# Optimization experiments

Measured on AMD Instinct MI355X. Metric: run time of the kernel, lower is better.

The kernel has to match this reference:

```python
import jax, jax.numpy as jnp
import numpy as np

B, S, HID, NH, HD = 2, 2048, 768, 12, 64
WINDOW = 128           # ModernBERT local attention window
ROPE_THETA = 10000.0   # local_rope_theta (layer_index=0 -> is_local_attention=True)


def _rotate_half(x):
    x1, x2 = jnp.split(x, 2, axis=-1)
    return jnp.concatenate([-x2, x1], axis=-1)


def setup_inputs() -> dict:
    key = jax.random.key(0)
    k1, k2, k3 = jax.random.split(key, 3)
    hidden_embed = jax.random.normal(k1, (B, S, HID), dtype=jnp.float32)
    Wq = jax.random.normal(k2, (HID, HID), dtype=jnp.float32) * (HID ** -0.5)
    Wo = jax.random.normal(k3, (HID, HID), dtype=jnp.float32) * (HID ** -0.5)
    position_index = jnp.arange(S, dtype=jnp.int32).reshape(1, S)
    # sliding-window additive mask: 0 inside window, -inf outside
    i = jnp.arange(S)
    dist = jnp.abs(i[:, None] - i[None, :])
    local_attention_mask = jnp.where(dist <= WINDOW // 2, 0.0, -jnp.inf).astype(jnp.float32)[None, None]
    global_attention_mask = jnp.zeros((1, 1, S, S), dtype=jnp.float32)
    return {
        "hidden_embed": hidden_embed,
        "Wq": Wq,
        "Wo": Wo,
        "local_attention_mask": local_attention_mask,
        "global_attention_mask": global_attention_mask,
        "position_index": position_index,
    }


def reference(hidden_embed, Wq, Wo, local_attention_mask, global_attention_mask, position_index):
    # q projection; NOTE: source has k = q.view(...), v = q.view(...) -> k and v ARE q
    q = hidden_embed @ Wq.T                                  # [B,S,HID]
    q = q.reshape(B, S, NH, HD).transpose(0, 2, 1, 3)        # [B,NH,S,HD]

    # RoPE
    inv_freq = 1.0 / (ROPE_THETA ** (jnp.arange(0, HD, 2, dtype=jnp.float32) / HD))  # [HD/2]
    pos = position_index.reshape(-1).astype(jnp.float32)     # [S]
    freqs = pos[:, None] * inv_freq[None, :]                 # [S,HD/2]
    emb = jnp.concatenate([freqs, freqs], axis=-1)           # [S,HD]
    cos, sin = jnp.cos(emb), jnp.sin(emb)
    q_rot = q * cos + _rotate_half(q) * sin                  # [B,NH,S,HD]
    k_rot = q_rot                                            # k == q before rope -> same after rope
    v = q                                                    # v == q (no rope on v)

    # masked SDPA (local layer -> local sliding-window mask)
    scale = jnp.asarray(HD, jnp.float32) ** -0.5
    scores = jnp.einsum('bhtd,bhsd->bhts', q_rot, k_rot) * scale + local_attention_mask
    attn = jax.nn.softmax(scores, axis=-1)                   # [B,NH,S,S]
    out = jnp.einsum('bhts,bhsd->bhtd', attn, v)             # [B,NH,S,HD]
    out = out.transpose(0, 2, 1, 3).reshape(B, S, HID)
    return out @ Wo.T
```

## Files before the change

### kernel.cpp

```cpp
#include <hip/hip_runtime.h>
#include <hip/hip_bf16.h>
#include <math.h>
#include <stdint.h>

#define B_    2
#define S_    2048
#define HID_  768
#define NH_   12
#define HD_   64
#define NROWS (B_ * S_)
#define N_HID_ELEM (NROWS * HID_)
#define N_W_ELEM   (HID_ * HID_)

#define KW   224
#define KSTR 232

#define TAB_ELEMS (S_ * 32)

typedef __bf16 bf16x8 __attribute__((ext_vector_type(8)));
typedef float  floatx4 __attribute__((ext_vector_type(4)));

__global__ void convert_inputs_kernel(const float* __restrict__ src_hidden,
                                      const float* __restrict__ src_w1,
                                      const float* __restrict__ src_w2,
                                      const int*   __restrict__ pos_idx,
                                      __hip_bfloat16* __restrict__ Hb,
                                      __hip_bfloat16* __restrict__ Wqb,
                                      __hip_bfloat16* __restrict__ Wob,
                                      float2* __restrict__ tab)
{
    int i = blockIdx.x * blockDim.x + threadIdx.x;
    const int NH4 = N_HID_ELEM / 4, NW4 = N_W_ELEM / 4;
    const int total4 = NH4 + 2 * NW4;
    if (i < total4) {
        const float* src;
        __hip_bfloat16* dst;
        int off;
        if (i < NH4)           { src = src_hidden; dst = Hb;  off = i; }
        else if (i < NH4+NW4)  { src = src_w1;     dst = Wqb; off = i - NH4; }
        else                   { src = src_w2;     dst = Wob; off = i - NH4 - NW4; }
        float4 v = reinterpret_cast<const float4*>(src)[off];
        __hip_bfloat16 o[4] = { __float2bfloat16(v.x), __float2bfloat16(v.y),
                                __float2bfloat16(v.z), __float2bfloat16(v.w) };
        *reinterpret_cast<uint64_t*>(dst + 4 * (size_t)off) = *reinterpret_cast<uint64_t*>(o);
    } else {
        int t = i - total4;
        if (t < TAB_ELEMS) {
            int s = t >> 5, f = t & 31;
            float inv = exp2f((float)f * (-0.41524101186092024f));
            float sn, cs;
            sincosf((float)pos_idx[s] * inv, &sn, &cs);
            tab[t] = make_float2(cs, sn);
        }
    }
}

__device__ __forceinline__ void gload_lds16(const __hip_bfloat16* g, __hip_bfloat16* l)
{
    __builtin_amdgcn_global_load_lds(
        (const __attribute__((address_space(1))) void*)g,
        (__attribute__((address_space(3))) void*)l, 16, 0, 0);
}

template<int ROPE>
__global__ __launch_bounds__(512) void gemm64k2(
    const __hip_bfloat16* __restrict__ A,
    const __hip_bfloat16* __restrict__ W,
    __hip_bfloat16* __restrict__ C,
    __hip_bfloat16* __restrict__ C2,
    float* __restrict__ Cf,
    const float2* __restrict__ tab,
    int M, int N, int K)
{
    __shared__ __align__(16) __hip_bfloat16 Ald[2][2][2][64][32];
    __shared__ __align__(16) __hip_bfloat16 Wld[2][2][2][64][32];

    const int tid  = threadIdx.x;
    const int kg   = tid >> 8;
    const int wv4  = (tid >> 6) & 3;
    const int lane = tid & 63;
    const int l16  = lane & 15;
    const int quad = lane >> 4;
    const int m0 = blockIdx.x * 64;
    const int n0 = blockIdx.y * 64;

    const int c    = wv4 * 64 + lane;
    const int sr   = c >> 2;
    const int sc8  = ((c & 3) ^ ((sr >> 1) & 3)) * 8;
    const int kbase = kg * 384;

    const __hip_bfloat16* gA = A + (size_t)(m0 + sr) * K + kbase + sc8;
    const __hip_bfloat16* gW = W + (size_t)(n0 + sr) * K + kbase + sc8;

    floatx4 acc[4] = {};
    const int ra  = wv4 * 16 + l16;
    const int qsw = (quad ^ ((l16 >> 1) & 3)) * 8;

#define STAGE(itx, buf) do {                                          \
        const int ko_ = (itx) * 64;                                   \
        gload_lds16(gA + ko_,      &Ald[kg][buf][0][wv4 * 16][0]);    \
        gload_lds16(gA + ko_ + 32, &Ald[kg][buf][1][wv4 * 16][0]);    \
        gload_lds16(gW + ko_,      &Wld[kg][buf][0][wv4 * 16][0]);    \
        gload_lds16(gW + ko_ + 32, &Wld[kg][buf][1][wv4 * 16][0]);    \
    } while (0)

    STAGE(0, 0);
    STAGE(1, 1);

#pragma unroll
    for (int it = 0; it < 6; ++it) {
        const int cur = it & 1;
        if (it == 5) { asm volatile("s_waitcnt vmcnt(0)" ::: "memory"); }
        else         { asm volatile("s_waitcnt vmcnt(4)" ::: "memory"); }
        __builtin_amdgcn_s_barrier();
        __builtin_amdgcn_sched_barrier(0);
#pragma unroll
        for (int ks = 0; ks < 2; ++ks) {
            bf16x8 a = *reinterpret_cast<const bf16x8*>(&Ald[kg][cur][ks][ra][qsw]);
#pragma unroll
            for (int u = 0; u < 4; ++u) {
                bf16x8 w = *reinterpret_cast<const bf16x8*>(
                    &Wld[kg][cur][ks][u * 16 + l16][qsw]);
                acc[u] = __builtin_amdgcn_mfma_f32_16x16x32_bf16(a, w, acc[u], 0, 0, 0);
            }
        }
        __builtin_amdgcn_sched_barrier(0);
        __builtin_amdgcn_s_barrier();
        if (it + 2 < 6) STAGE(it + 2, cur);
    }
#undef STAGE

    __syncthreads();
    float* Red = reinterpret_cast<float*>(&Ald[0][0][0][0][0]);
    if (kg == 1) {
#pragma unroll
        for (int u = 0; u < 4; ++u)
#pragma unroll
            for (int r = 0; r < 4; ++r)
                Red[(wv4 * 16 + quad * 4 + r) * 68 + u * 16 + l16] = acc[u][r];
    }
    __syncthreads();
    if (kg == 1) return;
#pragma unroll
    for (int u = 0; u < 4; ++u)
#pragma unroll
        for (int r = 0; r < 4; ++r)
            acc[u][r] += Red[(wv4 * 16 + quad * 4 + r) * 68 + u * 16 + l16];

    if (ROPE) {
#pragma unroll
        for (int r = 0; r < 4; ++r) {
            int m = m0 + wv4 * 16 + quad * 4 + r;
            int s = m & (S_ - 1);
#pragma unroll
            for (int u = 0; u < 2; ++u) {
                float2 cssn = tab[s * 32 + u * 16 + l16];
                float cs = cssn.x, sn = cssn.y;
                float q0 = acc[u][r];
                float q1 = acc[u + 2][r];
                size_t base = (size_t)m * HID_ + n0 + u * 16 + l16;
                C [base]      = __float2bfloat16(q0);
                C [base + 32] = __float2bfloat16(q1);
                C2[base]      = __float2bfloat16(q0 * cs - q1 * sn);
                C2[base + 32] = __float2bfloat16(q1 * cs + q0 * sn);
            }
        }
    } else {
#pragma unroll
        for (int u = 0; u < 4; ++u)
#pragma unroll
            for (int r = 0; r < 4; ++r) {
                int row = m0 + wv4 * 16 + quad * 4 + r;
                int col = n0 + u * 16 + l16;
                Cf[(size_t)row * N + col] = acc[u][r];
            }
    }
}

__global__ __launch_bounds__(256) void attn_kernel(
    const __hip_bfloat16* __restrict__ Q,
    const __hip_bfloat16* __restrict__ Qr,
    __hip_bfloat16* __restrict__ O)
{
    __shared__ __align__(16) __hip_bfloat16 Vt[64][KSTR];
    __shared__ __align__(16) __hip_bfloat16 KP[64 * KSTR];

    const int bh = blockIdx.y;
    const int b  = bh / NH_;
    const int h  = bh % NH_;
    const int i0 = blockIdx.x * 64;
    const int tid = threadIdx.x;

    if (tid < KW) {
        int j  = i0 - 64 + tid;
        int jc = min(max(j, 0), S_ - 1);
        const __hip_bfloat16* vrow = Q + ((size_t)(b * S_ + jc)) * HID_ + h * HD_;
#pragma unroll
        for (int d8i = 0; d8i < 8; ++d8i) {
            bf16x8 v = *reinterpret_cast<const bf16x8*>(vrow + d8i * 8);
            const __hip_bfloat16* ve = reinterpret_cast<const __hip_bfloat16*>(&v);
#pragma unroll
            for (int e = 0; e < 8; ++e) Vt[d8i * 8 + e][tid] = ve[e];
        }
    }

    {
        const int wvb = (tid >> 6) * 64;
        const int ln  = tid & 63;
#pragma unroll
        for (int i = 0; i < 7; ++i) {
            int cbase = i * 256 + wvb;
            int cc  = cbase + ln;
            int row = cc >> 3;
            int gp  = cc & 7;
            int gl  = gp ^ (row & 7);
            int j   = i0 - 64 + row;
            int jc  = min(max(j, 0), S_ - 1);
            gload_lds16(Qr + ((size_t)(b * S_ + jc)) * HID_ + h * HD_ + gl * 8,
                        KP + (size_t)cbase * 8);
        }
    }
    __syncthreads();

    const int wv   = tid >> 6;
    const int lane = tid & 63;
    const int l16  = lane & 15;
    const int quad = lane >> 4;

    floatx4 sc[10] = {};
    const __hip_bfloat16* qrow =
        Qr + ((size_t)(b * S_ + i0 + wv * 16 + l16)) * HID_ + h * HD_ + quad * 8;
    __builtin_amdgcn_s_setprio(1);
#pragma unroll
    for (int ks = 0; ks < 2; ++ks) {
        bf16x8 a = *reinterpret_cast<const bf16x8*>(qrow + ks * 32);
#pragma unroll
        for (int t = 0; t < 10; ++t) {
            int w  = (wv + t) * 16 + l16;
            int gp = ((ks * 4 + quad) ^ (w & 7)) * 8;
            bf16x8 bfr = *reinterpret_cast<const bf16x8*>(&KP[w * 64 + gp]);
            sc[t] = __builtin_amdgcn_mfma_f32_16x16x32_bf16(a, bfr, sc[t], 0, 0, 0);
        }
    }
    __builtin_amdgcn_s_setprio(0);
    __syncthreads();

    const float scale = 0.125f;
    float denom[4];
#pragma unroll
    for (int r = 0; r < 4; ++r) {
        const int R = wv * 16 + quad * 4 + r;
        float xv[10];
        float mx = -3.0e38f;
#pragma unroll
        for (int t = 0; t < 10; ++t) {
            int w = (wv + t) * 16 + l16;
            int j = i0 - 64 + w;
            bool valid = (w >= R) && (w <= R + 128) && (j >= 0) && (j < S_);
            float x = valid ? sc[t][r] * scale : -1.0e30f;
            xv[t] = x;
            mx = fmaxf(mx, x);
        }
#pragma unroll
        for (int msk = 1; msk < 16; msk <<= 1) mx = fmaxf(mx, __shfl_xor(mx, msk, 64));
        float sum = 0.f;
#pragma unroll
        for (int t = 0; t < 10; ++t) {
            float p = __expf(xv[t] - mx);
            sum += p;
            KP[R * KSTR + (wv + t) * 16 + l16] = __float2bfloat16(p);
        }
#pragma unroll
        for (int msk = 1; msk < 16; msk <<= 1) sum += __shfl_xor(sum, msk, 64);
        denom[r] = sum;
    }
    __syncthreads();

    floatx4 oacc[4] = {};
    __builtin_amdgcn_s_setprio(1);
#pragma unroll
    for (int c = 0; c < 5; ++c) {
        const int base = wv * 16 + c * 32;
        bf16x8 a = *reinterpret_cast<const bf16x8*>(
            &KP[(wv * 16 + l16) * KSTR + base + quad * 8]);
#pragma unroll
        for (int u = 0; u < 4; ++u) {
            bf16x8 bfr = *reinterpret_cast<const bf16x8*>(&Vt[u * 16 + l16][base + quad * 8]);
            oacc[u] = __builtin_amdgcn_mfma_f32_16x16x32_bf16(a, bfr, oacc[u], 0, 0, 0);
        }
    }
    __builtin_amdgcn_s_setprio(0);

    __syncthreads();
    float* Of = reinterpret_cast<float*>(&KP[0]);
#pragma unroll
    for (int u = 0; u < 4; ++u)
#pragma unroll
        for (int r = 0; r < 4; ++r)
            Of[(wv * 16 + quad * 4 + r) * 68 + u * 16 + l16] = oacc[u][r] / denom[r];
    __syncthreads();
    {
        int row = tid >> 2;
        int seg = (tid & 3) * 16;
        __hip_bfloat16 ob[16];
#pragma unroll
        for (int e = 0; e < 16; ++e)
            ob[e] = __float2bfloat16(Of[row * 68 + seg + e]);
        __hip_bfloat16* dst = O + ((size_t)(b * S_ + i0 + row)) * HID_ + h * HD_ + seg;
        *reinterpret_cast<bf16x8*>(dst)     = *reinterpret_cast<bf16x8*>(ob);
        *reinterpret_cast<bf16x8*>(dst + 8) = *reinterpret_cast<bf16x8*>(ob + 8);
    }
}

extern "C" void kernel_launch(void* const* d_in, const int* in_sizes, int n_in,
                              void* d_out, int out_size, void* d_ws, size_t ws_size,
                              hipStream_t stream)
{
    int ih = -1, iw1 = -1, iw2 = -1, ip = -1;
    for (int i = 0; i < n_in; ++i) {
        int s = in_sizes[i];
        if      (s == N_HID_ELEM && ih < 0) ih = i;
        else if (s == N_W_ELEM)  { if (iw1 < 0) iw1 = i; else if (iw2 < 0) iw2 = i; }
        else if (s == S_ && ip < 0) ip = i;
    }
    if (ih < 0)  ih = 0;
    if (iw1 < 0) iw1 = 1;
    if (iw2 < 0) iw2 = 2;
    if (ip < 0)  ip = 5;

    const float* hidden = (const float*)d_in[ih];
    const float* w1     = (const float*)d_in[iw1];
    const float* w2     = (const float*)d_in[iw2];
    const int*   pos    = (const int*)d_in[ip];

    __hip_bfloat16* Hb  = (__hip_bfloat16*)d_ws;
    __hip_bfloat16* Wqb = Hb  + N_HID_ELEM;
    __hip_bfloat16* Wob = Wqb + N_W_ELEM;
    __hip_bfloat16* Q   = Wob + N_W_ELEM;
    __hip_bfloat16* Qr  = Q   + N_HID_ELEM;
    float2*         Tab = reinterpret_cast<float2*>(Qr + N_HID_ELEM);
    __hip_bfloat16* AO  = Hb;

    int conv4 = (N_HID_ELEM + 2 * N_W_ELEM) / 4;
    int convtot = conv4 + TAB_ELEMS;
    convert_inputs_kernel<<<(convtot + 255) / 256, 256, 0, stream>>>(
        hidden, w1, w2, pos, Hb, Wqb, Wob, Tab);

    dim3 gblk(NROWS / 64, HID_ / 64);

    gemm64k2<1><<<gblk, 512, 0, stream>>>(Hb, Wqb, Q, Qr, nullptr, Tab,
                                          NROWS, HID_, HID_);

    attn_kernel<<<dim3(S_ / 64, B_ * NH_), 256, 0, stream>>>(Q, Qr, AO);

    gemm64k2<0><<<gblk, 512, 0, stream>>>(AO, Wob, nullptr, nullptr, (float*)d_out,
                                          nullptr, NROWS, HID_, HID_);
}
```

Measured before the change: 137.9 us.

## Fuse all stages into one cooperative persistent kernel with 128x64 GEMM tiles

Replaces the four separate launches (convert, QKV GEMM+RoPE, attention, output GEMM) with a single cooperative kernel of 384 blocks that uses grid.sync between stages, and falls back to separate launches if the cooperative launch fails. The GEMM tile is reworked from a 64x64 tile with a 2-way split-K reduction to a 128x64 tile over the full K with XOR-swizzled LDS, which removes the LDS reduction step. The aim is to cut launch gaps and the reduction cost. In exchange the kernel pays for grid-wide barriers, runs with fewer blocks per stage and may see lower occupancy from the larger shared-memory footprint.

```diff
diff --git a/kernel.cpp b/kernel.cpp
--- a/kernel.cpp
+++ b/kernel.cpp
@@ -1,7 +1,10 @@
 #include <hip/hip_runtime.h>
 #include <hip/hip_bf16.h>
+#include <hip/hip_cooperative_groups.h>
 #include <math.h>
 #include <stdint.h>
+
+namespace cg = cooperative_groups;
 
 #define B_    2
 #define S_    2048
@@ -17,35 +20,48 @@
 
 #define TAB_ELEMS (S_ * 32)
 
+#define GRID_FUSED 384
+
 typedef __bf16 bf16x8 __attribute__((ext_vector_type(8)));
 typedef float  floatx4 __attribute__((ext_vector_type(4)));
 
-__global__ void convert_inputs_kernel(const float* __restrict__ src_hidden,
-                                      const float* __restrict__ src_w1,
-                                      const float* __restrict__ src_w2,
-                                      const int*   __restrict__ pos_idx,
-                                      __hip_bfloat16* __restrict__ Hb,
-                                      __hip_bfloat16* __restrict__ Wqb,
-                                      __hip_bfloat16* __restrict__ Wob,
-                                      float2* __restrict__ tab)
-{
-    int i = blockIdx.x * blockDim.x + threadIdx.x;
+__device__ __forceinline__ void gload_lds16(const __hip_bfloat16* g, __hip_bfloat16* l)
+{
+    __builtin_amdgcn_global_load_lds(
+        (const __attribute__((address_space(1))) void*)g,
+        (__attribute__((address_space(3))) void*)l, 16, 0, 0);
+}
+
+__device__ __forceinline__ floatx4 mfma16(bf16x8 a, bf16x8 b, floatx4 c)
+{
+    return __builtin_amdgcn_mfma_f32_16x16x32_bf16(a, b, c, 0, 0, 0);
+}
+
+__device__ __forceinline__ void convert_body(
+    int gtid, int gstride,
+    const float* __restrict__ src_hidden, const float* __restrict__ src_w1,
+    const float* __restrict__ src_w2, const int* __restrict__ pos_idx,
+    __hip_bfloat16* __restrict__ Hb, __hip_bfloat16* __restrict__ Wqb,
+    __hip_bfloat16* __restrict__ Wob, float2* __restrict__ tab)
+{
     const int NH4 = N_HID_ELEM / 4, NW4 = N_W_ELEM / 4;
     const int total4 = NH4 + 2 * NW4;
-    if (i < total4) {
-        const float* src;
-        __hip_bfloat16* dst;
-        int off;
-        if (i < NH4)           { src = src_hidden; dst = Hb;  off = i; }
-        else if (i < NH4+NW4)  { src = src_w1;     dst = Wqb; off = i - NH4; }
-        else                   { src = src_w2;     dst = Wob; off = i - NH4 - NW4; }
-        float4 v = reinterpret_cast<const float4*>(src)[off];
-        __hip_bfloat16 o[4] = { __float2bfloat16(v.x), __float2bfloat16(v.y),
-                                __float2bfloat16(v.z), __float2bfloat16(v.w) };
-        *reinterpret_cast<uint64_t*>(dst + 4 * (size_t)off) = *reinterpret_cast<uint64_t*>(o);
-    } else {
-        int t = i - total4;
-        if (t < TAB_ELEMS) {
+    const int total  = total4 + TAB_ELEMS;
+    for (int i = gtid; i < total; i += gstride) {
+        if (i < total4) {
+            const float* src;
+            __hip_bfloat16* dst;
+            int off;
+            if (i < NH4)           { src = src_hidden; dst = Hb;  off = i; }
+            else if (i < NH4+NW4)  { src = src_w1;     dst = Wqb; off = i - NH4; }
+            else                   { src = src_w2;     dst = Wob; off = i - NH4 - NW4; }
+            float4 v = reinterpret_cast<const float4*>(src)[off];
+            __hip_bfloat16 o[4] = { __float2bfloat16(v.x), __float2bfloat16(v.y),
+                                    __float2bfloat16(v.z), __float2bfloat16(v.w) };
+            *reinterpret_cast<uint64_t*>(dst + 4 * (size_t)off) =
+                *reinterpret_cast<uint64_t*>(o);
+        } else {
+            int t = i - total4;
             int s = t >> 5, f = t & 31;
             float inv = exp2f((float)f * (-0.41524101186092024f));
             float sn, cs;
@@ -55,109 +71,98 @@
     }
 }
 
-__device__ __forceinline__ void gload_lds16(const __hip_bfloat16* g, __hip_bfloat16* l)
-{
-    __builtin_amdgcn_global_load_lds(
-        (const __attribute__((address_space(1))) void*)g,
-        (__attribute__((address_space(3))) void*)l, 16, 0, 0);
-}
-
 template<int ROPE>
-__global__ __launch_bounds__(512) void gemm64k2(
+__device__ __forceinline__ void gemm_tile(
     const __hip_bfloat16* __restrict__ A,
     const __hip_bfloat16* __restrict__ W,
     __hip_bfloat16* __restrict__ C,
     __hip_bfloat16* __restrict__ C2,
     float* __restrict__ Cf,
     const float2* __restrict__ tab,
-    int M, int N, int K)
-{
-    __shared__ __align__(16) __hip_bfloat16 Ald[2][2][2][64][32];
-    __shared__ __align__(16) __hip_bfloat16 Wld[2][2][2][64][32];
+    char* smem, int m0, int n0)
+{
+    constexpr int K = HID_;
+    auto Ald = reinterpret_cast<__hip_bfloat16(*)[128][64]>(smem);
+    auto Wld = reinterpret_cast<__hip_bfloat16(*)[64][64]>(smem + 32768);
 
     const int tid  = threadIdx.x;
-    const int kg   = tid >> 8;
-    const int wv4  = (tid >> 6) & 3;
+    const int wv   = tid >> 6;
     const int lane = tid & 63;
     const int l16  = lane & 15;
     const int quad = lane >> 4;
-    const int m0 = blockIdx.x * 64;
-    const int n0 = blockIdx.y * 64;
-
-    const int c    = wv4 * 64 + lane;
-    const int sr   = c >> 2;
-    const int sc8  = ((c & 3) ^ ((sr >> 1) & 3)) * 8;
-    const int kbase = kg * 384;
-
-    const __hip_bfloat16* gA = A + (size_t)(m0 + sr) * K + kbase + sc8;
-    const __hip_bfloat16* gW = W + (size_t)(n0 + sr) * K + kbase + sc8;
-
-    floatx4 acc[4] = {};
-    const int ra  = wv4 * 16 + l16;
-    const int qsw = (quad ^ ((l16 >> 1) & 3)) * 8;
-
-#define STAGE(itx, buf) do {                                          \
-        const int ko_ = (itx) * 64;                                   \
-        gload_lds16(gA + ko_,      &Ald[kg][buf][0][wv4 * 16][0]);    \
-        gload_lds16(gA + ko_ + 32, &Ald[kg][buf][1][wv4 * 16][0]);    \
-        gload_lds16(gW + ko_,      &Wld[kg][buf][0][wv4 * 16][0]);    \
-        gload_lds16(gW + ko_ + 32, &Wld[kg][buf][1][wv4 * 16][0]);    \
-    } while (0)
-
-    STAGE(0, 0);
-    STAGE(1, 1);
-
-#pragma unroll
-    for (int it = 0; it < 6; ++it) {
+
+    const int ch0 = wv * 64 + lane;
+    const __hip_bfloat16 *gA0, *gA1, *gA2, *gA3, *gW0, *gW1;
+    {
+        int ch, row, sp;
+        ch = ch0;        row = ch >> 3; sp = ch & 7;
+        gA0 = A + (size_t)(m0 + row) * K + ((sp ^ (row & 7)) << 3);
+        ch = 256 + ch0;  row = ch >> 3; sp = ch & 7;
+        gA1 = A + (size_t)(m0 + row) * K + ((sp ^ (row & 7)) << 3);
+        ch = 512 + ch0;  row = ch >> 3; sp = ch & 7;
+        gA2 = A + (size_t)(m0 + row) * K + ((sp ^ (row & 7)) << 3);
+        ch = 768 + ch0;  row = ch >> 3; sp = ch & 7;
+        gA3 = A + (size_t)(m0 + row) * K + ((sp ^ (row & 7)) << 3);
+        ch = ch0;        row = ch >> 3; sp = ch & 7;
+        gW0 = W + (size_t)(n0 + row) * K + ((sp ^ (row & 7)) << 3);
+        ch = 256 + ch0;  row = ch >> 3; sp = ch & 7;
+        gW1 = W + (size_t)(n0 + row) * K + ((sp ^ (row & 7)) << 3);
+    }
+
+    floatx4 acc[2][4] = {};
+
+    auto STG = [&](int itx, int buf) {
+        const int ko = itx * 64;
+        __hip_bfloat16* ab = &Ald[buf][0][0] + wv * 512;
+        __hip_bfloat16* wb = &Wld[buf][0][0] + wv * 512;
+        gload_lds16(gA0 + ko, ab);
+        gload_lds16(gA1 + ko, ab + 2048);
+        gload_lds16(gA2 + ko, ab + 4096);
+        gload_lds16(gA3 + ko, ab + 6144);
+        gload_lds16(gW0 + ko, wb);
+        gload_lds16(gW1 + ko, wb + 2048);
+    };
+
+    STG(0, 0);
+    STG(1, 1);
+
+#pragma unroll
+    for (int it = 0; it < 12; ++it) {
         const int cur = it & 1;
-        if (it == 5) { asm volatile("s_waitcnt vmcnt(0)" ::: "memory"); }
-        else         { asm volatile("s_waitcnt vmcnt(4)" ::: "memory"); }
+        if (it == 11) { asm volatile("s_waitcnt vmcnt(0)" ::: "memory"); }
+        else          { asm volatile("s_waitcnt vmcnt(6)" ::: "memory"); }
         __builtin_amdgcn_s_barrier();
         __builtin_amdgcn_sched_barrier(0);
 #pragma unroll
         for (int ks = 0; ks < 2; ++ks) {
-            bf16x8 a = *reinterpret_cast<const bf16x8*>(&Ald[kg][cur][ks][ra][qsw]);
+            const int gsw = ((ks * 4 + quad) ^ (l16 & 7)) * 8;
+            bf16x8 a0 = *reinterpret_cast<const bf16x8*>(&Ald[cur][wv * 32 + l16][gsw]);
+            bf16x8 a1 = *reinterpret_cast<const bf16x8*>(&Ald[cur][wv * 32 + 16 + l16][gsw]);
 #pragma unroll
             for (int u = 0; u < 4; ++u) {
-                bf16x8 w = *reinterpret_cast<const bf16x8*>(
-                    &Wld[kg][cur][ks][u * 16 + l16][qsw]);
-                acc[u] = __builtin_amdgcn_mfma_f32_16x16x32_bf16(a, w, acc[u], 0, 0, 0);
+                bf16x8 w = *reinterpret_cast<const bf16x8*>(&Wld[cur][u * 16 + l16][gsw]);
+                acc[0][u] = mfma16(a0, w, acc[0][u]);
+                acc[1][u] = mfma16(a1, w, acc[1][u]);
             }
         }
         __builtin_amdgcn_sched_barrier(0);
         __builtin_amdgcn_s_barrier();
-        if (it + 2 < 6) STAGE(it + 2, cur);
-    }
-#undef STAGE
-
-    __syncthreads();
-    float* Red = reinterpret_cast<float*>(&Ald[0][0][0][0][0]);
-    if (kg == 1) {
-#pragma unroll
-        for (int u = 0; u < 4; ++u)
-#pragma unroll
-            for (int r = 0; r < 4; ++r)
-                Red[(wv4 * 16 + quad * 4 + r) * 68 + u * 16 + l16] = acc[u][r];
-    }
-    __syncthreads();
-    if (kg == 1) return;
-#pragma unroll
-    for (int u = 0; u < 4; ++u)
-#pragma unroll
-        for (int r = 0; r < 4; ++r)
-            acc[u][r] += Red[(wv4 * 16 + quad * 4 + r) * 68 + u * 16 + l16];
+        if (it + 2 < 12) STG(it + 2, cur);
+    }
 
     if (ROPE) {
 #pragma unroll
+        for (int f = 0; f < 2; ++f)
+#pragma unroll
         for (int r = 0; r < 4; ++r) {
-            int m = m0 + wv4 * 16 + quad * 4 + r;
+            int m = m0 + wv * 32 + f * 16 + quad * 4 + r;
             int s = m & (S_ - 1);
 #pragma unroll
             for (int u = 0; u < 2; ++u) {
                 float2 cssn = tab[s * 32 + u * 16 + l16];
                 float cs = cssn.x, sn = cssn.y;
-                float q0 = acc[u][r];
-                float q1 = acc[u + 2][r];
+                float q0 = acc[f][u][r];
+                float q1 = acc[f][u + 2][r];
                 size_t base = (size_t)m * HID_ + n0 + u * 16 + l16;
                 C [base]      = __float2bfloat16(q0);
                 C [base + 32] = __float2bfloat16(q1);
@@ -167,28 +172,27 @@
         }
     } else {
 #pragma unroll
+        for (int f = 0; f < 2; ++f)
+#pragma unroll
         for (int u = 0; u < 4; ++u)
 #pragma unroll
             for (int r = 0; r < 4; ++r) {
-                int row = m0 + wv4 * 16 + quad * 4 + r;
+                int row = m0 + wv * 32 + f * 16 + quad * 4 + r;
                 int col = n0 + u * 16 + l16;
-                Cf[(size_t)row * N + col] = acc[u][r];
+                Cf[(size_t)row * HID_ + col] = acc[f][u][r];
             }
     }
 }
 
-__global__ __launch_bounds__(256) void attn_kernel(
+__device__ __forceinline__ void attn_tile(
     const __hip_bfloat16* __restrict__ Q,
     const __hip_bfloat16* __restrict__ Qr,
-    __hip_bfloat16* __restrict__ O)
-{
-    __shared__ __align__(16) __hip_bfloat16 Vt[64][KSTR];
-    __shared__ __align__(16) __hip_bfloat16 KP[64 * KSTR];
-
-    const int bh = blockIdx.y;
-    const int b  = bh / NH_;
-    const int h  = bh % NH_;
-    const int i0 = blockIdx.x * 64;
+    __hip_bfloat16* __restrict__ O,
+    char* smem, int b, int h, int i0)
+{
+    auto Vt = reinterpret_cast<__hip_bfloat16(*)[KSTR]>(smem);
+    __hip_bfloat16* KP = reinterpret_cast<__hip_bfloat16*>(smem + 64 * KSTR * 2);
+
     const int tid = threadIdx.x;
 
     if (tid < KW) {
@@ -239,7 +243,7 @@
             int w  = (wv + t) * 16 + l16;
             int gp = ((ks * 4 + quad) ^ (w & 7)) * 8;
             bf16x8 bfr = *reinterpret_cast<const bf16x8*>(&KP[w * 64 + gp]);
-            sc[t] = __builtin_amdgcn_mfma_f32_16x16x32_bf16(a, bfr, sc[t], 0, 0, 0);
+            sc[t] = mfma16(a, bfr, sc[t]);
         }
     }
     __builtin_amdgcn_s_setprio(0);
@@ -286,13 +290,13 @@
 #pragma unroll
         for (int u = 0; u < 4; ++u) {
             bf16x8 bfr = *reinterpret_cast<const bf16x8*>(&Vt[u * 16 + l16][base + quad * 8]);
-            oacc[u] = __builtin_amdgcn_mfma_f32_16x16x32_bf16(a, bfr, oacc[u], 0, 0, 0);
+            oacc[u] = mfma16(a, bfr, oacc[u]);
         }
     }
     __builtin_amdgcn_s_setprio(0);
 
     __syncthreads();
-    float* Of = reinterpret_cast<float*>(&KP[0]);
+    float* Of = reinterpret_cast<float*>(KP);
 #pragma unroll
     for (int u = 0; u < 4; ++u)
 #pragma unroll
@@ -312,6 +316,81 @@
     }
 }
 
+__global__ __launch_bounds__(256, 2) void fused_kernel(
+    const float* __restrict__ hidden, const float* __restrict__ w1,
+    const float* __restrict__ w2, const int* __restrict__ pos,
+    __hip_bfloat16* __restrict__ Hb, __hip_bfloat16* __restrict__ Wqb,
+    __hip_bfloat16* __restrict__ Wob, __hip_bfloat16* __restrict__ Q,
+    __hip_bfloat16* __restrict__ Qr, float2* __restrict__ Tab,
+    __hip_bfloat16* __restrict__ AO, float* __restrict__ out)
+{
+    __shared__ __align__(16) char smem[59392];
+    cg::grid_group grid = cg::this_grid();
+
+    convert_body(blockIdx.x * 256 + threadIdx.x, GRID_FUSED * 256,
+                 hidden, w1, w2, pos, Hb, Wqb, Wob, Tab);
+    grid.sync();
+
+    {
+        const int t = blockIdx.x;
+        gemm_tile<1>(Hb, Wqb, Q, Qr, nullptr, Tab, smem,
+                     (t & 31) * 128, (t >> 5) * 64);
+    }
+    grid.sync();
+
+#pragma unroll
+    for (int k = 0; k < 2; ++k) {
+        __syncthreads();
+        const int tt = blockIdx.x + k * GRID_FUSED;
+        const int i0 = (tt & 31) * 64;
+        const int bh = tt >> 5;
+        attn_tile(Q, Qr, AO, smem, bh / NH_, bh % NH_, i0);
+    }
+    grid.sync();
+
+    {
+        const int t = blockIdx.x;
+        gemm_tile<0>(AO, Wob, nullptr, nullptr, out, nullptr, smem,
+                     (t & 31) * 128, (t >> 5) * 64);
+    }
+}
+
+__global__ void convert_fb(const float* __restrict__ h, const float* __restrict__ w1,
+                           const float* __restrict__ w2, const int* __restrict__ pos,
+                           __hip_bfloat16* __restrict__ Hb, __hip_bfloat16* __restrict__ Wqb,
+                           __hip_bfloat16* __restrict__ Wob, float2* __restrict__ tab)
+{
+    convert_body(blockIdx.x * blockDim.x + threadIdx.x, gridDim.x * blockDim.x,
+                 h, w1, w2, pos, Hb, Wqb, Wob, tab);
+}
+
+__global__ __launch_bounds__(256) void gemm1_fb(
+    const __hip_bfloat16* __restrict__ A, const __hip_bfloat16* __restrict__ W,
+    __hip_bfloat16* __restrict__ C, __hip_bfloat16* __restrict__ C2,
+    const float2* __restrict__ tab)
+{
+    __shared__ __align__(16) char smem[49152];
+    const int t = blockIdx.x;
+    gemm_tile<1>(A, W, C, C2, nullptr, tab, smem, (t & 31) * 128, (t >> 5) * 64);
+}
+
+__global__ __launch_bounds__(256) void gemm2_fb(
+    const __hip_bfloat16* __restrict__ A, const __hip_bfloat16* __restrict__ W,
+    float* __restrict__ out)
+{
+    __shared__ __align__(16) char smem[49152];
+    const int t = blockIdx.x;
+    gemm_tile<0>(A, W, nullptr, nullptr, out, nullptr, smem, (t & 31) * 128, (t >> 5) * 64);
+}
+
+__global__ __launch_bounds__(256) void attn_fb(
+    const __hip_bfloat16* __restrict__ Q, const __hip_bfloat16* __restrict__ Qr,
+    __hip_bfloat16* __restrict__ O)
+{
+    __shared__ __align__(16) char smem[59392];
+    attn_tile(Q, Qr, O, smem, blockIdx.y / NH_, blockIdx.y % NH_, blockIdx.x * 64);
+}
+
 extern "C" void kernel_launch(void* const* d_in, const int* in_sizes, int n_in,
                               void* d_out, int out_size, void* d_ws, size_t ws_size,
                               hipStream_t stream)
@@ -340,19 +419,21 @@
     __hip_bfloat16* Qr  = Q   + N_HID_ELEM;
     float2*         Tab = reinterpret_cast<float2*>(Qr + N_HID_ELEM);
     __hip_bfloat16* AO  = Hb;
-
-    int conv4 = (N_HID_ELEM + 2 * N_W_ELEM) / 4;
-    int convtot = conv4 + TAB_ELEMS;
-    convert_inputs_kernel<<<(convtot + 255) / 256, 256, 0, stream>>>(
-        hidden, w1, w2, pos, Hb, Wqb, Wob, Tab);
-
-    dim3 gblk(NROWS / 64, HID_ / 64);
-
-    gemm64k2<1><<<gblk, 512, 0, stream>>>(Hb, Wqb, Q, Qr, nullptr, Tab,
-                                          NROWS, HID_, HID_);
-
-    attn_kernel<<<dim3(S_ / 64, B_ * NH_), 256, 0, stream>>>(Q, Qr, AO);
-
-    gemm64k2<0><<<gblk, 512, 0, stream>>>(AO, Wob, nullptr, nullptr, (float*)d_out,
-                                          nullptr, NROWS, HID_, HID_);
-}
+    float*          outp = (float*)d_out;
+
+    void* args[12] = { (void*)&hidden, (void*)&w1, (void*)&w2, (void*)&pos,
+                       (void*)&Hb, (void*)&Wqb, (void*)&Wob, (void*)&Q,
+                       (void*)&Qr, (void*)&Tab, (void*)&AO, (void*)&outp };
+
+    hipError_t e = hipLaunchCooperativeKernel((const void*)fused_kernel,
+                                              dim3(GRID_FUSED), dim3(256),
+                                              args, 0, stream);
+    if (e != hipSuccess) {
+        int conv4 = (N_HID_ELEM + 2 * N_W_ELEM) / 4 + TAB_ELEMS;
+        convert_fb<<<(conv4 + 255) / 256, 256, 0, stream>>>(
+            hidden, w1, w2, pos, Hb, Wqb, Wob, Tab);
+        gemm1_fb<<<GRID_FUSED, 256, 0, stream>>>(Hb, Wqb, Q, Qr, Tab);
+        attn_fb<<<dim3(S_ / 64, B_ * NH_), 256, 0, stream>>>(Q, Qr, AO);
+        gemm2_fb<<<GRID_FUSED, 256, 0, stream>>>(AO, Wob, outp);
+    }
+}
```

Measured after the change: 298.2 us. 116% more time.

## Drop intra-block split-K in GEMMs, use 256-thread blocks with full K loop

Applied to the files above, without the earlier changes.

Removes the two-way split-K within each GEMM block (512 threads, two K halves reduced through LDS) and replaces it with 256-thread blocks that each loop over the full K in 12 double-buffered stages. This eliminates the LDS reduction and its extra barriers and halves the shared memory per block, with launch bounds hinting at higher occupancy. In exchange each block has a longer serial K loop and fewer waves in flight per tile to hide load latency.

```diff
diff --git a/kernel.cpp b/kernel.cpp
--- a/kernel.cpp
+++ b/kernel.cpp
@@ -63,7 +63,7 @@
 }
 
 template<int ROPE>
-__global__ __launch_bounds__(512) void gemm64k2(
+__global__ __launch_bounds__(256, 5) void gemm64ns(
     const __hip_bfloat16* __restrict__ A,
     const __hip_bfloat16* __restrict__ W,
     __hip_bfloat16* __restrict__ C,
@@ -72,85 +72,66 @@
     const float2* __restrict__ tab,
     int M, int N, int K)
 {
-    __shared__ __align__(16) __hip_bfloat16 Ald[2][2][2][64][32];
-    __shared__ __align__(16) __hip_bfloat16 Wld[2][2][2][64][32];
+    __shared__ __align__(16) __hip_bfloat16 Ald[2][2][64][32];
+    __shared__ __align__(16) __hip_bfloat16 Wld[2][2][64][32];
 
     const int tid  = threadIdx.x;
-    const int kg   = tid >> 8;
-    const int wv4  = (tid >> 6) & 3;
+    const int wv   = tid >> 6;
     const int lane = tid & 63;
     const int l16  = lane & 15;
     const int quad = lane >> 4;
     const int m0 = blockIdx.x * 64;
     const int n0 = blockIdx.y * 64;
 
-    const int c    = wv4 * 64 + lane;
+    const int c    = wv * 64 + lane;
     const int sr   = c >> 2;
     const int sc8  = ((c & 3) ^ ((sr >> 1) & 3)) * 8;
-    const int kbase = kg * 384;
-
-    const __hip_bfloat16* gA = A + (size_t)(m0 + sr) * K + kbase + sc8;
-    const __hip_bfloat16* gW = W + (size_t)(n0 + sr) * K + kbase + sc8;
+
+    const __hip_bfloat16* gA = A + (size_t)(m0 + sr) * K + sc8;
+    const __hip_bfloat16* gW = W + (size_t)(n0 + sr) * K + sc8;
 
     floatx4 acc[4] = {};
-    const int ra  = wv4 * 16 + l16;
+    const int ra  = wv * 16 + l16;
     const int qsw = (quad ^ ((l16 >> 1) & 3)) * 8;
 
-#define STAGE(itx, buf) do {                                          \
-        const int ko_ = (itx) * 64;                                   \
-        gload_lds16(gA + ko_,      &Ald[kg][buf][0][wv4 * 16][0]);    \
-        gload_lds16(gA + ko_ + 32, &Ald[kg][buf][1][wv4 * 16][0]);    \
-        gload_lds16(gW + ko_,      &Wld[kg][buf][0][wv4 * 16][0]);    \
-        gload_lds16(gW + ko_ + 32, &Wld[kg][buf][1][wv4 * 16][0]);    \
+#define STAGE(itx, buf) do {                                      \
+        const int ko_ = (itx) * 64;                               \
+        gload_lds16(gA + ko_,      &Ald[buf][0][wv * 16][0]);     \
+        gload_lds16(gA + ko_ + 32, &Ald[buf][1][wv * 16][0]);     \
+        gload_lds16(gW + ko_,      &Wld[buf][0][wv * 16][0]);     \
+        gload_lds16(gW + ko_ + 32, &Wld[buf][1][wv * 16][0]);     \
     } while (0)
 
     STAGE(0, 0);
     STAGE(1, 1);
 
 #pragma unroll
-    for (int it = 0; it < 6; ++it) {
+    for (int it = 0; it < 12; ++it) {
         const int cur = it & 1;
-        if (it == 5) { asm volatile("s_waitcnt vmcnt(0)" ::: "memory"); }
-        else         { asm volatile("s_waitcnt vmcnt(4)" ::: "memory"); }
+        if (it == 11) { asm volatile("s_waitcnt vmcnt(0)" ::: "memory"); }
+        else          { asm volatile("s_waitcnt vmcnt(4)" ::: "memory"); }
         __builtin_amdgcn_s_barrier();
         __builtin_amdgcn_sched_barrier(0);
 #pragma unroll
         for (int ks = 0; ks < 2; ++ks) {
-            bf16x8 a = *reinterpret_cast<const bf16x8*>(&Ald[kg][cur][ks][ra][qsw]);
+            bf16x8 a = *reinterpret_cast<const bf16x8*>(&Ald[cur][ks][ra][qsw]);
 #pragma unroll
             for (int u = 0; u < 4; ++u) {
                 bf16x8 w = *reinterpret_cast<const bf16x8*>(
-                    &Wld[kg][cur][ks][u * 16 + l16][qsw]);
+                    &Wld[cur][ks][u * 16 + l16][qsw]);
                 acc[u] = __builtin_amdgcn_mfma_f32_16x16x32_bf16(a, w, acc[u], 0, 0, 0);
             }
         }
         __builtin_amdgcn_sched_barrier(0);
         __builtin_amdgcn_s_barrier();
-        if (it + 2 < 6) STAGE(it + 2, cur);
+        if (it + 2 < 12) STAGE(it + 2, cur);
     }
 #undef STAGE
 
-    __syncthreads();
-    float* Red = reinterpret_cast<float*>(&Ald[0][0][0][0][0]);
-    if (kg == 1) {
-#pragma unroll
-        for (int u = 0; u < 4; ++u)
-#pragma unroll
-            for (int r = 0; r < 4; ++r)
-                Red[(wv4 * 16 + quad * 4 + r) * 68 + u * 16 + l16] = acc[u][r];
-    }
-    __syncthreads();
-    if (kg == 1) return;
-#pragma unroll
-    for (int u = 0; u < 4; ++u)
-#pragma unroll
-        for (int r = 0; r < 4; ++r)
-            acc[u][r] += Red[(wv4 * 16 + quad * 4 + r) * 68 + u * 16 + l16];
-
     if (ROPE) {
 #pragma unroll
         for (int r = 0; r < 4; ++r) {
-            int m = m0 + wv4 * 16 + quad * 4 + r;
+            int m = m0 + wv * 16 + quad * 4 + r;
             int s = m & (S_ - 1);
 #pragma unroll
             for (int u = 0; u < 2; ++u) {
@@ -170,7 +151,7 @@
         for (int u = 0; u < 4; ++u)
 #pragma unroll
             for (int r = 0; r < 4; ++r) {
-                int row = m0 + wv4 * 16 + quad * 4 + r;
+                int row = m0 + wv * 16 + quad * 4 + r;
                 int col = n0 + u * 16 + l16;
                 Cf[(size_t)row * N + col] = acc[u][r];
             }
@@ -348,11 +329,11 @@
 
     dim3 gblk(NROWS / 64, HID_ / 64);
 
-    gemm64k2<1><<<gblk, 512, 0, stream>>>(Hb, Wqb, Q, Qr, nullptr, Tab,
+    gemm64ns<1><<<gblk, 256, 0, stream>>>(Hb, Wqb, Q, Qr, nullptr, Tab,
                                           NROWS, HID_, HID_);
 
     attn_kernel<<<dim3(S_ / 64, B_ * NH_), 256, 0, stream>>>(Q, Qr, AO);
 
-    gemm64k2<0><<<gblk, 512, 0, stream>>>(AO, Wob, nullptr, nullptr, (float*)d_out,
+    gemm64ns<0><<<gblk, 256, 0, stream>>>(AO, Wob, nullptr, nullptr, (float*)d_out,
                                           nullptr, NROWS, HID_, HID_);
 }
```

Measured after the change: 136.6 us. About the same (-0.9%).
